# Performance work log

Measured on AMD Instinct MI355X. Metric: run time of the kernel, lower is better.

## Reference

```python
import jax, jax.numpy as jnp
import numpy as np

D_MODEL = 1024
N_HEADS = 16
D_K = D_MODEL // N_HEADS


def _xavier(key, shape):
    fan_in, fan_out = shape[1], shape[0]
    a = np.sqrt(6.0 / (fan_in + fan_out))
    return jax.random.uniform(key, shape, jnp.float32, -a, a)


def setup_inputs() -> dict:
    key = jax.random.key(0)
    kx, kq, kk, kv, ko = jax.random.split(key, 5)
    x = jax.random.normal(kx, (2, 2048, D_MODEL), jnp.float32)
    # nn.Linear weights are [out, in]; y = x @ W.T
    Wq = _xavier(kq, (D_MODEL, D_MODEL))
    Wk = _xavier(kk, (D_MODEL, D_MODEL))
    Wv = _xavier(kv, (D_MODEL, D_MODEL))
    Wo = _xavier(ko, (D_MODEL, D_MODEL))
    bo = jnp.zeros((D_MODEL,), jnp.float32)
    return {"x": x, "Wq": Wq, "Wk": Wk, "Wv": Wv, "Wo": Wo, "bo": bo}


def reference(x, Wq, Wk, Wv, Wo, bo):
    B, S, D = x.shape
    def split_heads(t):
        # [B,S,D] -> [B,H,S,d_k]
        return t.reshape(B, S, N_HEADS, D_K).transpose(0, 2, 1, 3)
    Q = split_heads(x @ Wq.T)
    K = split_heads(x @ Wk.T)
    V = split_heads(x @ Wv.T)
    scale = 1.0 / jnp.sqrt(jnp.asarray(D_K, x.dtype))
    scores = jnp.einsum('bhqd,bhkd->bhqk', Q, K) * scale  # [B,H,S,S]
    attn = jax.nn.softmax(scores, axis=-1)
    out = jnp.einsum('bhqk,bhkd->bhqd', attn, V)  # [B,H,S,d_k]
    out = out.transpose(0, 2, 1, 3).reshape(B, S, D)  # merge heads
    return out @ Wo.T + bo
```

## Files before the change

kernel.cpp:

```cpp
#include <hip/hip_runtime.h>


typedef __attribute__((ext_vector_type(8))) short bf16x8;
typedef __attribute__((ext_vector_type(4))) short bf16x4;
typedef __attribute__((ext_vector_type(4))) float f32x4;
typedef __attribute__((ext_vector_type(2))) unsigned int u32x2;
typedef __attribute__((ext_vector_type(4))) unsigned int u32x4;

#define GK 1024
#define SEQ 2048
#define NHEAD 16
#define DKD 64
#define PADW 72

#define MFMA32(a, b, c) __builtin_amdgcn_mfma_f32_16x16x32_bf16((a), (b), (c), 0, 0, 0)

#if __has_builtin(__builtin_amdgcn_exp2f)
#define EXP2(x) __builtin_amdgcn_exp2f(x)
#else
#define EXP2(x) exp2f(x)
#endif

#define QSCALE 0.18033688011f

static __device__ __forceinline__ unsigned short f2bf(float f) {
    unsigned int u = __float_as_uint(f);
    u += 0x7fffu + ((u >> 16) & 1u);
    return (unsigned short)(u >> 16);
}

static __device__ __forceinline__ unsigned int pack_bf2(float a, float b) {
    unsigned int ua = __float_as_uint(a) + 0x8000u;
    unsigned int ub = __float_as_uint(b) + 0x8000u;
    return __builtin_amdgcn_perm(ub, ua, 0x07060302u);
}

__global__ __launch_bounds__(256) void cast_all(const float* __restrict__ x,
                                                const float* __restrict__ wq,
                                                const float* __restrict__ wk,
                                                const float* __restrict__ wv,
                                                const float* __restrict__ wo,
                                                unsigned short* __restrict__ Xb,
                                                unsigned short* __restrict__ Wqkv,
                                                unsigned short* __restrict__ Wob) {
    const int bid = blockIdx.x;
    const float* src; unsigned short* dst; int off;
    if (bid < 4096)      { src = x;  dst = Xb;             off = bid; }
    else if (bid < 5120) { src = wq; dst = Wqkv;           off = bid - 4096; }
    else if (bid < 6144) { src = wk; dst = Wqkv + 1048576; off = bid - 5120; }
    else if (bid < 7168) { src = wv; dst = Wqkv + 2097152; off = bid - 6144; }
    else                 { src = wo; dst = Wob;            off = bid - 7168; }
    const int i = off * 1024 + threadIdx.x * 4;
    float4 v = *(const float4*)(src + i);
    u32x2 p; p.x = pack_bf2(v.x, v.y); p.y = pack_bf2(v.z, v.w);
    *(u32x2*)(dst + i) = p;
}

template <int MODE, int BN>
__global__ __launch_bounds__(256) void gemm_bt(const unsigned short* __restrict__ A,
                                               const unsigned short* __restrict__ Bw,
                                               unsigned short* __restrict__ outb,
                                               float* __restrict__ outf,
                                               const float* __restrict__ bias) {
    constexpr int NJ = BN / 32;
    constexpr int LOOP_BYTES = 128 * 64 * 2 + BN * 64 * 2;
    constexpr int EPI_BYTES  = 4 * 64 * PADW * 2;
    constexpr int SMEM_BYTES = (MODE == 0)
        ? (LOOP_BYTES > EPI_BYTES ? LOOP_BYTES : EPI_BYTES)
        : LOOP_BYTES;
    __shared__ __align__(16) unsigned char SMEM[SMEM_BYTES];
    unsigned short* As = (unsigned short*)SMEM;
    unsigned short* Bs = As + 128 * 64;

    const int t    = threadIdx.x;
    const int lane = t & 63;
    const int w    = t >> 6;
    const int wm   = (w >> 1) * 64;
    const int wn   = (w & 1) * (BN / 2);
    const int bm0  = blockIdx.x * 128;
    const int bn0  = blockIdx.y * BN;
    const int lm   = lane & 15;
    const int lq   = lane >> 4;
    const int swzb = lm & 7;

    const unsigned short* Ab = A + (size_t)bm0 * GK;
    const unsigned short* Bb = Bw + (size_t)bn0 * GK;

    f32x4 acc[4][NJ];
    const f32x4 Z4 = {0.f, 0.f, 0.f, 0.f};
#pragma unroll
    for (int i = 0; i < 4; i++)
#pragma unroll
        for (int j = 0; j < NJ; j++) acc[i][j] = Z4;

    const int q_uni = (t & ~63);

    for (int k0 = 0; k0 < GK; k0 += 64) {
        __syncthreads();
#pragma unroll
        for (int i = 0; i < 4; ++i) {
            int q  = i * 256 + t;
            int r  = q >> 3;
            int gc = (q & 7) ^ (r & 7);
            int q0 = i * 256 + q_uni;
            __builtin_amdgcn_global_load_lds(
                (const __attribute__((address_space(1))) void*)(Ab + (size_t)r * GK + k0 + gc * 8),
                (__attribute__((address_space(3))) void*)(As + (size_t)q0 * 8),
                16, 0, 0);
        }
#pragma unroll
        for (int i = 0; i < BN / 32; ++i) {
            int q  = i * 256 + t;
            int r  = q >> 3;
            int gc = (q & 7) ^ (r & 7);
            int q0 = i * 256 + q_uni;
            __builtin_amdgcn_global_load_lds(
                (const __attribute__((address_space(1))) void*)(Bb + (size_t)r * GK + k0 + gc * 8),
                (__attribute__((address_space(3))) void*)(Bs + (size_t)q0 * 8),
                16, 0, 0);
        }
        __syncthreads();

#pragma unroll
        for (int kk = 0; kk < 2; ++kk) {
            const int swz = ((kk * 4 + lq) ^ swzb) * 8;
            bf16x8 af[4], bf[NJ];
#pragma unroll
            for (int i = 0; i < 4; i++)
                af[i] = *(const bf16x8*)(As + (wm + i * 16 + lm) * 64 + swz);
#pragma unroll
            for (int j = 0; j < NJ; j++)
                bf[j] = *(const bf16x8*)(Bs + (wn + j * 16 + lm) * 64 + swz);
#pragma unroll
            for (int i = 0; i < 4; i++)
#pragma unroll
                for (int j = 0; j < NJ; j++)
                    acc[i][j] = MFMA32(af[i], bf[j], acc[i][j]);
        }
    }

    if (MODE == 0) {
        __syncthreads();
        unsigned short* E  = (unsigned short*)SMEM;
        unsigned short* Ew = E + w * (64 * PADW);
        const int nbase = bn0 + wn;
        const int which = nbase >> 10;
        const int hh    = (nbase & 1023) >> 6;
        if (which != 2) {
            const float sc = (which == 0) ? QSCALE : 1.0f;
#pragma unroll
            for (int i = 0; i < 4; i++)
#pragma unroll
                for (int j = 0; j < 4; j++)
#pragma unroll
                    for (int r = 0; r < 4; r++)
                        Ew[(i * 16 + lq * 4 + r) * PADW + j * 16 + lm] =
                            f2bf(acc[i][j][r] * sc);
            unsigned short* dst = outb + (size_t)which * 4194304;
#pragma unroll
            for (int rep = 0; rep < 8; ++rep) {
                const int mm = rep * 8 + (lane >> 3);
                const int d0 = (lane & 7) * 8;
                uint4 v = *(const uint4*)(Ew + mm * PADW + d0);
                const int m_g = bm0 + wm + mm;
                const int b = m_g >> 11, s = m_g & 2047;
                *(uint4*)(dst + (((size_t)(b * NHEAD + hh)) * SEQ + s) * DKD + d0) = v;
            }
        } else {
#pragma unroll
            for (int i = 0; i < 4; i++)
#pragma unroll
                for (int j = 0; j < 4; j++) {
                    u32x2 pk;
                    pk.x = pack_bf2(acc[i][j][0], acc[i][j][1]);
                    pk.y = pack_bf2(acc[i][j][2], acc[i][j][3]);
                    *(u32x2*)(Ew + (j * 16 + lm) * PADW + i * 16 + lq * 4) = pk;
                }
            unsigned short* dst = outb + (size_t)2 * 4194304;
#pragma unroll
            for (int rep = 0; rep < 8; ++rep) {
                const int nn = rep * 8 + (lane >> 3);
                const int mc = (lane & 7) * 8;
                uint4 v = *(const uint4*)(Ew + nn * PADW + mc);
                const int m_g = bm0 + wm + mc;
                const int b = m_g >> 11, s0 = m_g & 2047;
                *(uint4*)(dst + (((size_t)(b * NHEAD + hh)) * DKD + nn) * SEQ + s0) = v;
            }
        }
    } else {
#pragma unroll
        for (int i = 0; i < 4; i++) {
            const int mbase = bm0 + wm + i * 16 + lq * 4;
#pragma unroll
            for (int j = 0; j < NJ; j++) {
                const int n = bn0 + wn + j * 16 + lm;
#pragma unroll
                for (int r = 0; r < 4; r++)
                    outf[(size_t)(mbase + r) * 1024 + n] = acc[i][j][r] + bias[n];
            }
        }
    }
}

__global__ __launch_bounds__(256, 3) void attn_kernel(const unsigned short* __restrict__ Qg,
                                                      const unsigned short* __restrict__ Kg,
                                                      const unsigned short* __restrict__ Vtg,
                                                      unsigned short* __restrict__ Og) {
    __shared__ __align__(16) unsigned short KV[2][2][64 * PADW];

    const int id  = blockIdx.x;
    const int xcd = id & 7;
    const int j8  = id >> 3;
    const int bh  = xcd * 4 + (j8 & 3);
    const int qb  = j8 >> 2;
    const unsigned short* Qp  = Qg  + ((size_t)bh * SEQ + qb * 64) * DKD;
    const unsigned short* Kp  = Kg  + (size_t)bh * SEQ * DKD;
    const unsigned short* Vtp = Vtg + (size_t)bh * DKD * SEQ;

    const int t    = threadIdx.x;
    const int lane = t & 63;
    const int w    = t >> 6;
    const int lm   = lane & 15;
    const int kq   = lane >> 4;

    const f32x4 Z4 = {0.f, 0.f, 0.f, 0.f};

    bf16x8 aq[4][2];
#pragma unroll
    for (int c = 0; c < 4; ++c)
#pragma unroll
        for (int kk = 0; kk < 2; ++kk)
            aq[c][kk] = *(const bf16x8*)(Qp + (size_t)(c * 16 + lm) * DKD + kk * 32 + kq * 8);

    f32x4 o[4][4];
    float ls[4];
#pragma unroll
    for (int c = 0; c < 4; ++c) {
        ls[c] = 0.f;
#pragma unroll
        for (int dj = 0; dj < 4; ++dj) o[c][dj] = Z4;
    }

    const int sr = t >> 2, sc = (t & 3) * 16;
    uint4 kreg0, kreg1, vreg0, vreg1;
    {
        const unsigned short* kp = Kp + (size_t)sr * DKD + sc;
        const unsigned short* vp = Vtp + (size_t)sr * SEQ + sc;
        uint4 a0 = *(const uint4*)(kp), a1 = *(const uint4*)(kp + 8);
        uint4 b0 = *(const uint4*)(vp), b1 = *(const uint4*)(vp + 8);
        uint4* dk = (uint4*)(&KV[0][0][sr * PADW + sc]); dk[0] = a0; dk[1] = a1;
        uint4* dv = (uint4*)(&KV[0][1][sr * PADW + sc]); dv[0] = b0; dv[1] = b1;
    }
    {
        const unsigned short* kp = Kp + (size_t)(64 + sr) * DKD + sc;
        kreg0 = *(const uint4*)(kp); kreg1 = *(const uint4*)(kp + 8);
        const unsigned short* vp = Vtp + (size_t)sr * SEQ + 64 + sc;
        vreg0 = *(const uint4*)(vp); vreg1 = *(const uint4*)(vp + 8);
    }

    u32x2 pkE[4], bvE[4];

#pragma unroll 1
    for (int p = 0; p < 16; ++p) {
        {
            const int kt = 2 * p;
            __syncthreads();
            {
                uint4* dk = (uint4*)(&KV[1][0][sr * PADW + sc]);
                dk[0] = kreg0; dk[1] = kreg1;
                uint4* dv = (uint4*)(&KV[1][1][sr * PADW + sc]);
                dv[0] = vreg0; dv[1] = vreg1;
            }
            if (kt + 2 < 32) {
                const unsigned short* kp = Kp + (size_t)((kt + 2) * 64 + sr) * DKD + sc;
                kreg0 = *(const uint4*)(kp); kreg1 = *(const uint4*)(kp + 8);
                const unsigned short* vp = Vtp + (size_t)sr * SEQ + (kt + 2) * 64 + sc;
                vreg0 = *(const uint4*)(vp); vreg1 = *(const uint4*)(vp + 8);
            }
            const unsigned short* Kc = &KV[0][0][0];
            const unsigned short* Vc = &KV[0][1][0];

            bf16x8 ak0 = *(const bf16x8*)(Kc + (w * 16 + lm) * PADW + kq * 8);
            bf16x8 ak1 = *(const bf16x8*)(Kc + (w * 16 + lm) * PADW + 32 + kq * 8);
            f32x4 s[4];
#pragma unroll
            for (int c = 0; c < 4; ++c) {
                s[c] = MFMA32(ak0, aq[c][0], Z4);
                s[c] = MFMA32(ak1, aq[c][1], s[c]);
            }
#pragma unroll
            for (int c = 0; c < 4; ++c) {
#pragma unroll
                for (int r = 0; r < 4; ++r) s[c][r] = EXP2(s[c][r]);
                ls[c] += (s[c][0] + s[c][1]) + (s[c][2] + s[c][3]);
                pkE[c].x = pack_bf2(s[c][0], s[c][1]);
                pkE[c].y = pack_bf2(s[c][2], s[c][3]);
            }
#pragma unroll
            for (int dj = 0; dj < 4; ++dj)
                bvE[dj] = __builtin_bit_cast(u32x2,
                    *(const bf16x4*)(Vc + (dj * 16 + lm) * PADW + w * 16 + kq * 4));
        }

        {
            const int kt = 2 * p + 1;
            __syncthreads();
            if (kt + 1 < 32) {
                uint4* dk = (uint4*)(&KV[0][0][sr * PADW + sc]);
                dk[0] = kreg0; dk[1] = kreg1;
                uint4* dv = (uint4*)(&KV[0][1][sr * PADW + sc]);
                dv[0] = vreg0; dv[1] = vreg1;
            }
            if (kt + 2 < 32) {
                const unsigned short* kp = Kp + (size_t)((kt + 2) * 64 + sr) * DKD + sc;
                kreg0 = *(const uint4*)(kp); kreg1 = *(const uint4*)(kp + 8);
                const unsigned short* vp = Vtp + (size_t)sr * SEQ + (kt + 2) * 64 + sc;
                vreg0 = *(const uint4*)(vp); vreg1 = *(const uint4*)(vp + 8);
            }
            const unsigned short* Kc = &KV[1][0][0];
            const unsigned short* Vc = &KV[1][1][0];

            bf16x8 ak0 = *(const bf16x8*)(Kc + (w * 16 + lm) * PADW + kq * 8);
            bf16x8 ak1 = *(const bf16x8*)(Kc + (w * 16 + lm) * PADW + 32 + kq * 8);
            f32x4 s[4];
#pragma unroll
            for (int c = 0; c < 4; ++c) {
                s[c] = MFMA32(ak0, aq[c][0], Z4);
                s[c] = MFMA32(ak1, aq[c][1], s[c]);
            }
            u32x2 pkO[4];
#pragma unroll
            for (int c = 0; c < 4; ++c) {
#pragma unroll
                for (int r = 0; r < 4; ++r) s[c][r] = EXP2(s[c][r]);
                ls[c] += (s[c][0] + s[c][1]) + (s[c][2] + s[c][3]);
                pkO[c].x = pack_bf2(s[c][0], s[c][1]);
                pkO[c].y = pack_bf2(s[c][2], s[c][3]);
            }

#pragma unroll
            for (int dj = 0; dj < 4; ++dj) {
                u32x2 bvO = __builtin_bit_cast(u32x2,
                    *(const bf16x4*)(Vc + (dj * 16 + lm) * PADW + w * 16 + kq * 4));
                u32x4 bw; bw.x = bvE[dj].x; bw.y = bvE[dj].y; bw.z = bvO.x; bw.w = bvO.y;
                bf16x8 bv = __builtin_bit_cast(bf16x8, bw);
#pragma unroll
                for (int c = 0; c < 4; ++c) {
                    u32x4 aw; aw.x = pkE[c].x; aw.y = pkE[c].y; aw.z = pkO[c].x; aw.w = pkO[c].y;
                    bf16x8 av = __builtin_bit_cast(bf16x8, aw);
                    o[c][dj] = MFMA32(av, bv, o[c][dj]);
                }
            }
        }
    }

    __syncthreads();
    float* Lf = (float*)(&KV[0][0][0]);

#pragma unroll
    for (int c = 0; c < 4; ++c) {
        float v = ls[c];
        v += __shfl_xor(v, 16);
        v += __shfl_xor(v, 32);
        if (kq == 0) Lf[w * 64 + c * 16 + lm] = v;
    }
    __syncthreads();

    const int rq = t >> 2;
    const int dq = (t & 3) * 8;
    float li = (Lf[rq] + Lf[64 + rq]) + (Lf[128 + rq] + Lf[192 + rq]);
#if __has_builtin(__builtin_amdgcn_rcpf)
    li = __builtin_amdgcn_rcpf(li);
#else
    li = 1.0f / li;
#endif
    __syncthreads();

    const int b = bh >> 4, h = bh & 15;
#pragma unroll
    for (int p = 0; p < 2; ++p) {
#pragma unroll
        for (int c = 0; c < 4; ++c)
#pragma unroll
            for (int djh = 0; djh < 2; ++djh) {
                const int dj = 2 * p + djh;
#pragma unroll
                for (int r = 0; r < 4; ++r)
                    Lf[(w * 64 + c * 16 + kq * 4 + r) * 36 + djh * 16 + lm] = o[c][dj][r];
            }
        __syncthreads();
        f32x4 a0 = Z4, a1 = Z4;
#pragma unroll
        for (int wp = 0; wp < 4; ++wp) {
            a0 += *(const f32x4*)(Lf + (wp * 64 + rq) * 36 + dq);
            a1 += *(const f32x4*)(Lf + (wp * 64 + rq) * 36 + dq + 4);
        }
        uint4 outv;
        outv.x = pack_bf2(a0[0] * li, a0[1] * li);
        outv.y = pack_bf2(a0[2] * li, a0[3] * li);
        outv.z = pack_bf2(a1[0] * li, a1[1] * li);
        outv.w = pack_bf2(a1[2] * li, a1[3] * li);
        *(uint4*)(Og + (((size_t)(b * SEQ + qb * 64 + rq)) * NHEAD + h) * DKD + p * 32 + dq) = outv;
        __syncthreads();
    }
}

extern "C" void kernel_launch(void* const* d_in, const int* in_sizes, int n_in,
                              void* d_out, int out_size, void* d_ws, size_t ws_size,
                              hipStream_t stream) {
    const float* x  = (const float*)d_in[0];
    const float* Wq = (const float*)d_in[1];
    const float* Wk = (const float*)d_in[2];
    const float* Wv = (const float*)d_in[3];
    const float* Wo = (const float*)d_in[4];
    const float* bo = (const float*)d_in[5];
    float* out = (float*)d_out;

    unsigned short* ws = (unsigned short*)d_ws;
    unsigned short* Xb   = ws;
    unsigned short* Wqkv = ws + 4194304;
    unsigned short* Wob  = ws + 7340032;
    unsigned short* QKV  = ws + 8388608;
    unsigned short* Ob   = ws + 20971520;

    cast_all<<<8192, 256, 0, stream>>>(x, Wq, Wk, Wv, Wo, Xb, Wqkv, Wob);
    gemm_bt<0, 128><<<dim3(32, 24), 256, 0, stream>>>(Xb, Wqkv, QKV, nullptr, nullptr);
    attn_kernel<<<1024, 256, 0, stream>>>(QKV, QKV + 4194304, QKV + 8388608, Ob);
    gemm_bt<1, 64><<<dim3(32, 16), 256, 0, stream>>>(Ob, Wob, nullptr, out, bo);
}
```

Measured before the change: 213.1 us.

## Load K fragments directly from global into registers and use per-tile 16x16x16 PV MFMAs

K tiles are no longer staged through shared memory. Each wave loads its K MFMA fragments straight from global into registers, prefetched two tiles ahead, so only V goes through LDS. The PV product now uses 16x16x16 MFMAs on each tile instead of pairing even and odd tiles into 16x16x32 MFMAs, so the cross-tile register state goes away. The unroll-1 pragma on the outer loop is also removed. The aim is less LDS traffic and store work per iteration, in exchange for twice as many smaller PV MFMAs and uncoalesced-style fragment loads from global.

```diff
diff --git a/kernel.cpp b/kernel.cpp
--- a/kernel.cpp
+++ b/kernel.cpp
@@ -5,7 +5,6 @@
 typedef __attribute__((ext_vector_type(4))) short bf16x4;
 typedef __attribute__((ext_vector_type(4))) float f32x4;
 typedef __attribute__((ext_vector_type(2))) unsigned int u32x2;
-typedef __attribute__((ext_vector_type(4))) unsigned int u32x4;
 
 #define GK 1024
 #define SEQ 2048
@@ -14,6 +13,7 @@
 #define PADW 72
 
 #define MFMA32(a, b, c) __builtin_amdgcn_mfma_f32_16x16x32_bf16((a), (b), (c), 0, 0, 0)
+#define MFMA16(a, b, c) __builtin_amdgcn_mfma_f32_16x16x16bf16_1k((a), (b), (c), 0, 0, 0)
 
 #if __has_builtin(__builtin_amdgcn_exp2f)
 #define EXP2(x) __builtin_amdgcn_exp2f(x)
@@ -242,115 +242,114 @@
     }
 
     const int sr = t >> 2, sc = (t & 3) * 16;
-    uint4 kreg0, kreg1, vreg0, vreg1;
+    uint4 vreg0, vreg1;
     {
-        const unsigned short* kp = Kp + (size_t)sr * DKD + sc;
         const unsigned short* vp = Vtp + (size_t)sr * SEQ + sc;
-        uint4 a0 = *(const uint4*)(kp), a1 = *(const uint4*)(kp + 8);
         uint4 b0 = *(const uint4*)(vp), b1 = *(const uint4*)(vp + 8);
-        uint4* dk = (uint4*)(&KV[0][0][sr * PADW + sc]); dk[0] = a0; dk[1] = a1;
         uint4* dv = (uint4*)(&KV[0][1][sr * PADW + sc]); dv[0] = b0; dv[1] = b1;
     }
     {
-        const unsigned short* kp = Kp + (size_t)(64 + sr) * DKD + sc;
-        kreg0 = *(const uint4*)(kp); kreg1 = *(const uint4*)(kp + 8);
         const unsigned short* vp = Vtp + (size_t)sr * SEQ + 64 + sc;
         vreg0 = *(const uint4*)(vp); vreg1 = *(const uint4*)(vp + 8);
     }
 
-    u32x2 pkE[4], bvE[4];
-
-#pragma unroll 1
+    const unsigned short* Kfrag = Kp + (size_t)(w * 16 + lm) * DKD + kq * 8;
+    bf16x8 akA0 = *(const bf16x8*)(Kfrag);
+    bf16x8 akA1 = *(const bf16x8*)(Kfrag + 32);
+    bf16x8 akB0 = *(const bf16x8*)(Kfrag + 64 * DKD);
+    bf16x8 akB1 = *(const bf16x8*)(Kfrag + 64 * DKD + 32);
+
     for (int p = 0; p < 16; ++p) {
         {
             const int kt = 2 * p;
             __syncthreads();
+            f32x4 s[4];
+#pragma unroll
+            for (int c = 0; c < 4; ++c) {
+                s[c] = MFMA32(akA0, aq[c][0], Z4);
+                s[c] = MFMA32(akA1, aq[c][1], s[c]);
+            }
+            const unsigned short* Vc = &KV[0][1][0];
+            bf16x4 bv[4];
+#pragma unroll
+            for (int dj = 0; dj < 4; ++dj)
+                bv[dj] = *(const bf16x4*)(Vc + (dj * 16 + lm) * PADW + w * 16 + kq * 4);
             {
-                uint4* dk = (uint4*)(&KV[1][0][sr * PADW + sc]);
-                dk[0] = kreg0; dk[1] = kreg1;
                 uint4* dv = (uint4*)(&KV[1][1][sr * PADW + sc]);
                 dv[0] = vreg0; dv[1] = vreg1;
             }
             if (kt + 2 < 32) {
-                const unsigned short* kp = Kp + (size_t)((kt + 2) * 64 + sr) * DKD + sc;
-                kreg0 = *(const uint4*)(kp); kreg1 = *(const uint4*)(kp + 8);
                 const unsigned short* vp = Vtp + (size_t)sr * SEQ + (kt + 2) * 64 + sc;
                 vreg0 = *(const uint4*)(vp); vreg1 = *(const uint4*)(vp + 8);
-            }
-            const unsigned short* Kc = &KV[0][0][0];
-            const unsigned short* Vc = &KV[0][1][0];
-
-            bf16x8 ak0 = *(const bf16x8*)(Kc + (w * 16 + lm) * PADW + kq * 8);
-            bf16x8 ak1 = *(const bf16x8*)(Kc + (w * 16 + lm) * PADW + 32 + kq * 8);
-            f32x4 s[4];
-#pragma unroll
-            for (int c = 0; c < 4; ++c) {
-                s[c] = MFMA32(ak0, aq[c][0], Z4);
-                s[c] = MFMA32(ak1, aq[c][1], s[c]);
-            }
+                const unsigned short* kf = Kfrag + (size_t)(kt + 2) * 64 * DKD;
+                akA0 = *(const bf16x8*)(kf); akA1 = *(const bf16x8*)(kf + 32);
+            }
+
 #pragma unroll
             for (int c = 0; c < 4; ++c) {
 #pragma unroll
                 for (int r = 0; r < 4; ++r) s[c][r] = EXP2(s[c][r]);
                 ls[c] += (s[c][0] + s[c][1]) + (s[c][2] + s[c][3]);
-                pkE[c].x = pack_bf2(s[c][0], s[c][1]);
-                pkE[c].y = pack_bf2(s[c][2], s[c][3]);
+            }
+            bf16x4 ap[4];
+#pragma unroll
+            for (int c = 0; c < 4; ++c) {
+                u32x2 pk;
+                pk.x = pack_bf2(s[c][0], s[c][1]);
+                pk.y = pack_bf2(s[c][2], s[c][3]);
+                ap[c] = __builtin_bit_cast(bf16x4, pk);
             }
 #pragma unroll
             for (int dj = 0; dj < 4; ++dj)
-                bvE[dj] = __builtin_bit_cast(u32x2,
-                    *(const bf16x4*)(Vc + (dj * 16 + lm) * PADW + w * 16 + kq * 4));
+#pragma unroll
+                for (int c = 0; c < 4; ++c)
+                    o[c][dj] = MFMA16(ap[c], bv[dj], o[c][dj]);
         }
 
         {
             const int kt = 2 * p + 1;
             __syncthreads();
+            f32x4 s[4];
+#pragma unroll
+            for (int c = 0; c < 4; ++c) {
+                s[c] = MFMA32(akB0, aq[c][0], Z4);
+                s[c] = MFMA32(akB1, aq[c][1], s[c]);
+            }
+            const unsigned short* Vc = &KV[1][1][0];
+            bf16x4 bv[4];
+#pragma unroll
+            for (int dj = 0; dj < 4; ++dj)
+                bv[dj] = *(const bf16x4*)(Vc + (dj * 16 + lm) * PADW + w * 16 + kq * 4);
             if (kt + 1 < 32) {
-                uint4* dk = (uint4*)(&KV[0][0][sr * PADW + sc]);
-                dk[0] = kreg0; dk[1] = kreg1;
                 uint4* dv = (uint4*)(&KV[0][1][sr * PADW + sc]);
                 dv[0] = vreg0; dv[1] = vreg1;
             }
             if (kt + 2 < 32) {
-                const unsigned short* kp = Kp + (size_t)((kt + 2) * 64 + sr) * DKD + sc;
-                kreg0 = *(const uint4*)(kp); kreg1 = *(const uint4*)(kp + 8);
                 const unsigned short* vp = Vtp + (size_t)sr * SEQ + (kt + 2) * 64 + sc;
                 vreg0 = *(const uint4*)(vp); vreg1 = *(const uint4*)(vp + 8);
-            }
-            const unsigned short* Kc = &KV[1][0][0];
-            const unsigned short* Vc = &KV[1][1][0];
-
-            bf16x8 ak0 = *(const bf16x8*)(Kc + (w * 16 + lm) * PADW + kq * 8);
-            bf16x8 ak1 = *(const bf16x8*)(Kc + (w * 16 + lm) * PADW + 32 + kq * 8);
-            f32x4 s[4];
-#pragma unroll
-            for (int c = 0; c < 4; ++c) {
-                s[c] = MFMA32(ak0, aq[c][0], Z4);
-                s[c] = MFMA32(ak1, aq[c][1], s[c]);
-            }
-            u32x2 pkO[4];
+                const unsigned short* kf = Kfrag + (size_t)(kt + 2) * 64 * DKD;
+                akB0 = *(const bf16x8*)(kf); akB1 = *(const bf16x8*)(kf + 32);
+            }
+
 #pragma unroll
             for (int c = 0; c < 4; ++c) {
 #pragma unroll
                 for (int r = 0; r < 4; ++r) s[c][r] = EXP2(s[c][r]);
                 ls[c] += (s[c][0] + s[c][1]) + (s[c][2] + s[c][3]);
-                pkO[c].x = pack_bf2(s[c][0], s[c][1]);
-                pkO[c].y = pack_bf2(s[c][2], s[c][3]);
-            }
-
-#pragma unroll
-            for (int dj = 0; dj < 4; ++dj) {
-                u32x2 bvO = __builtin_bit_cast(u32x2,
-                    *(const bf16x4*)(Vc + (dj * 16 + lm) * PADW + w * 16 + kq * 4));
-                u32x4 bw; bw.x = bvE[dj].x; bw.y = bvE[dj].y; bw.z = bvO.x; bw.w = bvO.y;
-                bf16x8 bv = __builtin_bit_cast(bf16x8, bw);
-#pragma unroll
-                for (int c = 0; c < 4; ++c) {
-                    u32x4 aw; aw.x = pkE[c].x; aw.y = pkE[c].y; aw.z = pkO[c].x; aw.w = pkO[c].y;
-                    bf16x8 av = __builtin_bit_cast(bf16x8, aw);
-                    o[c][dj] = MFMA32(av, bv, o[c][dj]);
-                }
-            }
+            }
+            bf16x4 ap[4];
+#pragma unroll
+            for (int c = 0; c < 4; ++c) {
+                u32x2 pk;
+                pk.x = pack_bf2(s[c][0], s[c][1]);
+                pk.y = pack_bf2(s[c][2], s[c][3]);
+                ap[c] = __builtin_bit_cast(bf16x4, pk);
+            }
+#pragma unroll
+            for (int dj = 0; dj < 4; ++dj)
+#pragma unroll
+                for (int c = 0; c < 4; ++c)
+                    o[c][dj] = MFMA16(ap[c], bv[dj], o[c][dj]);
         }
     }
 
```

Result: slower. 229.4 us (+7.7%).
